# Performance work log

Measured on AMD Instinct MI355X. Metric: run time of the kernel, lower is better.

The kernel has to match this reference:

```python
import jax, jax.numpy as jnp
import numpy as np

EMBED_DIM = 2048
NUM_HEADS = 16
HEAD_DIM = EMBED_DIM // NUM_HEADS  # 128


def setup_inputs() -> dict:
    key = jax.random.key(0)
    ks = jax.random.split(key, 11)
    B, S, D, Hd = 2, 2048, EMBED_DIM, HEAD_DIM
    s_in = 1.0 / np.sqrt(D)
    return {
        "query": jax.random.normal(ks[0], (B, S, D), dtype=jnp.float32),
        "key": jax.random.normal(ks[1], (B, S, D), dtype=jnp.float32),
        "value": jax.random.normal(ks[2], (B, S, D), dtype=jnp.float32),
        "Wq": jax.random.normal(ks[3], (D, D), dtype=jnp.float32) * s_in,
        "bq": jax.random.normal(ks[4], (D,), dtype=jnp.float32) * s_in,
        "Wk": jax.random.normal(ks[5], (D, Hd), dtype=jnp.float32) * s_in,
        "bk": jax.random.normal(ks[6], (Hd,), dtype=jnp.float32) * s_in,
        "Wv": jax.random.normal(ks[7], (D, Hd), dtype=jnp.float32) * s_in,
        "bv": jax.random.normal(ks[8], (Hd,), dtype=jnp.float32) * s_in,
        "Wo": jax.random.normal(ks[9], (D, D), dtype=jnp.float32) * s_in,
        "bo": jax.random.normal(ks[10], (D,), dtype=jnp.float32) * s_in,
    }


def reference(query, key, value, Wq, bq, Wk, bk, Wv, bv, Wo, bo):
    B, S, D = query.shape
    H, Hd = NUM_HEADS, HEAD_DIM
    # projections
    Q = (query @ Wq + bq).reshape(B, S, H, Hd).transpose(0, 2, 1, 3)  # [B,H,S,Hd]
    K = key @ Wk + bk    # [B,S,Hd] single shared KV head
    V = value @ Wv + bv  # [B,S,Hd]
    scale = 1.0 / jnp.sqrt(jnp.asarray(Hd, dtype=Q.dtype))
    # MQA: broadcast single K/V head across H query heads
    scores = jnp.einsum("bhsd,btd->bhst", Q, K) * scale  # [B,H,S,S]
    attn = jax.nn.softmax(scores, axis=-1)
    out = jnp.einsum("bhst,btd->bhsd", attn, V)  # [B,H,S,Hd]
    out = out.transpose(0, 2, 1, 3).reshape(B, S, D)
    return out @ Wo + bo
```

## Files before the change

kernel.cpp:

```cpp
#include <hip/hip_runtime.h>
#include <stdint.h>

#define S_LEN 2048
#define EMBED 2048
#define NHEADS 16
#define HDIM 128

typedef __attribute__((ext_vector_type(8))) short bf16x8;
typedef __attribute__((ext_vector_type(4))) float f32x4;
typedef unsigned short us;

static __device__ __forceinline__ us f2b(float f) {
    union { float f; unsigned u; } x; x.f = f;
    unsigned r = x.u + 0x7fffu + ((x.u >> 16) & 1u);
    return (us)(r >> 16);
}

static __device__ __forceinline__ uint2 pack4(float a, float b, float c, float d) {
    uint2 u;
    u.x = (unsigned)f2b(a) | ((unsigned)f2b(b) << 16);
    u.y = (unsigned)f2b(c) | ((unsigned)f2b(d) << 16);
    return u;
}

static __device__ __forceinline__ void gl_lds16(const void* g, void* l) {
    __builtin_amdgcn_global_load_lds(
        (const __attribute__((address_space(1))) void*)g,
        (__attribute__((address_space(3))) void*)l, 16, 0, 0);
}


static __device__ __forceinline__ void dma_tile(const us* __restrict__ g, int k0,
                                                us* dst, int tid) {
#pragma unroll
    for (int i = 0; i < 4; i++) {
        int sl = i * 256 + tid;
        int row = sl >> 3, cp = sl & 7, c = cp ^ (row & 7);
        gl_lds16(g + (size_t)row * 2048 + k0 + c * 8,
                 (char*)dst + (i * 256 + (tid & 192)) * 16);
    }
}

static __device__ __forceinline__ void loadA_f32(const float* __restrict__ g,
                                                 float4 pf[8]) {
#pragma unroll
    for (int i = 0; i < 8; i++) pf[i] = ((const float4*)g)[i];
}

static __device__ __forceinline__ void writeA_f32(us* dst, const float4 pf[8],
                                                  int row, int h) {
#pragma unroll
    for (int cc = 0; cc < 4; cc++) {
        int p = (h * 4 + cc) ^ (row & 7);
        float4 a = pf[cc * 2], b = pf[cc * 2 + 1];
        uint4 u;
        u.x = (unsigned)f2b(a.x) | ((unsigned)f2b(a.y) << 16);
        u.y = (unsigned)f2b(a.z) | ((unsigned)f2b(a.w) << 16);
        u.z = (unsigned)f2b(b.x) | ((unsigned)f2b(b.y) << 16);
        u.w = (unsigned)f2b(b.z) | ((unsigned)f2b(b.w) << 16);
        *(uint4*)&dst[row * 64 + p * 8] = u;
    }
}

static __device__ __forceinline__ void frag_mfma(const us* curA, const us* curB,
                                                 int wm, int wn, int lm, int quad,
                                                 f32x4 acc[4][4]) {
#pragma unroll
    for (int kc = 0; kc < 2; kc++) {
        bf16x8 af[4], bfr[4];
#pragma unroll
        for (int mi = 0; mi < 4; mi++) {
            int row = wm * 64 + mi * 16 + lm;
            int p = (kc * 4 + quad) ^ (row & 7);
            af[mi] = *(const bf16x8*)&curA[row * 64 + p * 8];
        }
#pragma unroll
        for (int ni = 0; ni < 4; ni++) {
            int row = wn * 64 + ni * 16 + lm;
            int p = (kc * 4 + quad) ^ (row & 7);
            bfr[ni] = *(const bf16x8*)&curB[row * 64 + p * 8];
        }
#pragma unroll
        for (int mi = 0; mi < 4; mi++)
#pragma unroll
            for (int ni = 0; ni < 4; ni++)
                acc[mi][ni] = __builtin_amdgcn_mfma_f32_16x16x32_bf16(
                    af[mi], bfr[ni], acc[mi][ni], 0, 0, 0);
    }
}

__global__ void tcast3(const float* __restrict__ Wq, const float* __restrict__ Wk,
                       const float* __restrict__ Wv, const float* __restrict__ query,
                       us* __restrict__ Wqt, us* __restrict__ Wkvt,
                       us* __restrict__ qbf) {
    int b = blockIdx.x;
    if (b >= 2304) {
        int id = (b - 2304) * 256 + threadIdx.x;
        const float4* in4 = (const float4*)query;
        float4 a = in4[id * 2], c = in4[id * 2 + 1];
        uint4 u;
        u.x = (unsigned)f2b(a.x) | ((unsigned)f2b(a.y) << 16);
        u.y = (unsigned)f2b(a.z) | ((unsigned)f2b(a.w) << 16);
        u.z = (unsigned)f2b(c.x) | ((unsigned)f2b(c.y) << 16);
        u.w = (unsigned)f2b(c.z) | ((unsigned)f2b(c.w) << 16);
        ((uint4*)qbf)[id] = u;
        return;
    }
    const float* in; us* out; int N, rel;
    if (b < 2048)      { in = Wq; out = Wqt;  N = 2048; rel = b; }
    else if (b < 2176) { in = Wk; out = Wkvt; N = 128;  rel = b - 2048; }
    else               { in = Wv; out = Wkvt + (size_t)128 * 2048; N = 128; rel = b - 2176; }
    int id = rel * 256 + threadIdx.x;
    int n = id & (N - 1), k0 = (id / N) * 8;
    us t8[8];
#pragma unroll
    for (int j = 0; j < 8; j++) t8[j] = f2b(in[(size_t)(k0 + j) * N + n]);
    *(uint4*)&out[(size_t)n * 2048 + k0] = *(uint4*)t8;
}

__global__ __launch_bounds__(256, 2) void proj_qkv(
    const float* __restrict__ key, const float* __restrict__ value,
    const us* __restrict__ qbf, const us* __restrict__ Wqt,
    const us* __restrict__ Wkvt, const float* __restrict__ bq,
    us* __restrict__ Qh, float* __restrict__ part)
{
    __shared__ __align__(16) us A0[128 * 64], A1[128 * 64];
    __shared__ __align__(16) us B0[128 * 64], B1[128 * 64];

    const int tid = threadIdx.x;
    const int lane = tid & 63, w = tid >> 6, lm = lane & 15, quad = lane >> 4;
    const int wm = w >> 1, wn = w & 1;
    const int id = blockIdx.x;

    f32x4 acc[4][4];
#pragma unroll
    for (int i = 0; i < 4; i++)
#pragma unroll
        for (int j = 0; j < 4; j++) acc[i][j] = (f32x4){0.f, 0.f, 0.f, 0.f};

    if (id < 512) {
        const int bn = (id & 15) * 128, bm = (id >> 4) * 128;
        const us* Atile = qbf + (size_t)bm * 2048;
        const us* Btile = Wqt + (size_t)bn * 2048;

        dma_tile(Atile, 0, A0, tid);
        dma_tile(Btile, 0, B0, tid);

        for (int kk = 0; kk < 32; kk += 2) {
            __syncthreads();
            if (kk + 1 < 32) { dma_tile(Atile, (kk + 1) * 64, A1, tid);
                               dma_tile(Btile, (kk + 1) * 64, B1, tid); }
            frag_mfma(A0, B0, wm, wn, lm, quad, acc);
            __syncthreads();
            if (kk + 2 < 32) { dma_tile(Atile, (kk + 2) * 64, A0, tid);
                               dma_tile(Btile, (kk + 2) * 64, B0, tid); }
            frag_mfma(A1, B1, wm, wn, lm, quad, acc);
        }

#pragma unroll
        for (int mi = 0; mi < 4; mi++)
#pragma unroll
            for (int ni = 0; ni < 4; ni++) {
                int col = bn + wn * 64 + ni * 16 + lm;
                float bv = bq[col];
#pragma unroll
                for (int r = 0; r < 4; r++) {
                    int row = bm + wm * 64 + mi * 16 + quad * 4 + r;
                    float v = acc[mi][ni][r] + bv;
                    int b = row >> 11, s = row & 2047;
                    int hh = col >> 7, hd = col & 127;
                    size_t addr = (((size_t)(b * 16 + hh) * 2048 + s) << 7)
                                  + (((hd >> 3) ^ (s & 7)) << 3) + (hd & 7);
                    Qh[addr] = f2b(v);
                }
            }
    } else {
        int e = id - 512;
        int z = e >> 6, r = e & 63, isV = r & 1;
        int bm = (r >> 1) * 128, bn = isV * 128;
        const float* Atile = (isV ? value : key) + (size_t)bm * 2048;
        const us* Btile = Wkvt + (size_t)bn * 2048;
        const int kbeg = z * 512, iters = 8;
        const int arow = tid >> 1, h = tid & 1;
        const float* Ag = Atile + (size_t)arow * 2048 + h * 32;

        float4 pf[8];
        loadA_f32(Ag + kbeg, pf);
        dma_tile(Btile, kbeg, B0, tid);
        writeA_f32(A0, pf, arow, h);

        for (int kk = 0; kk < iters; kk += 2) {
            const int k1 = kbeg + (kk + 1) * 64;
            const int k2 = kbeg + (kk + 2) * 64;
            __syncthreads();
            if (kk + 1 < iters) { loadA_f32(Ag + k1, pf); dma_tile(Btile, k1, B1, tid); }
            frag_mfma(A0, B0, wm, wn, lm, quad, acc);
            if (kk + 1 < iters) writeA_f32(A1, pf, arow, h);
            __syncthreads();
            if (kk + 2 < iters) { loadA_f32(Ag + k2, pf); dma_tile(Btile, k2, B0, tid); }
            frag_mfma(A1, B1, wm, wn, lm, quad, acc);
            if (kk + 2 < iters) writeA_f32(A0, pf, arow, h);
        }

        float* pp = part + (size_t)z * 1048576;
#pragma unroll
        for (int mi = 0; mi < 4; mi++)
#pragma unroll
            for (int ni = 0; ni < 4; ni++) {
                int col = bn + wn * 64 + ni * 16 + lm;
#pragma unroll
                for (int r = 0; r < 4; r++) {
                    int row = bm + wm * 64 + mi * 16 + quad * 4 + r;
                    pp[(size_t)row * 256 + col] = acc[mi][ni][r];
                }
            }
    }
}

__global__ void finish_wot(const float* __restrict__ part, const float* __restrict__ bk,
                           const float* __restrict__ bv, us* __restrict__ Kb,
                           us* __restrict__ Vt, const float* __restrict__ Wo,
                           us* __restrict__ Wot) {
    int b = blockIdx.x;
    if (b < 2048) {
        int id = b * 256 + threadIdx.x;
        int n = id & 2047, k0 = (id >> 11) * 8;
        us t8[8];
#pragma unroll
        for (int j = 0; j < 8; j++) t8[j] = f2b(Wo[(size_t)(k0 + j) * 2048 + n]);
        *(uint4*)&Wot[(size_t)n * 2048 + k0] = *(uint4*)t8;
    } else {
        int id = (b - 2048) * 256 + threadIdx.x;
        int row = id >> 8, n = id & 255;
        float s = part[id] + part[1048576 + id] + part[2097152 + id] + part[3145728 + id];
        int bb = row >> 11, t = row & 2047;
        if (n < 128) {
            int hd = n;
            s += bk[hd];
            Kb[((size_t)(bb * 2048 + t) << 7) + (((hd >> 3) ^ (t & 7)) << 3) + (hd & 7)] = f2b(s);
        } else {
            int hd = n - 128;
            s += bv[hd];
            size_t addr = (((size_t)(bb * 64 + (t >> 5)) * 128 + hd) << 5)
                          + ((((t >> 3) & 3) ^ ((hd >> 1) & 3)) << 3) + (t & 7);
            Vt[addr] = f2b(s);
        }
    }
}

__global__ __launch_bounds__(256, 2) void mqa_attn(
    const us* __restrict__ Qh, const us* __restrict__ Kb,
    const us* __restrict__ Vt, us* __restrict__ AO)
{
    __shared__ __align__(16) char smem[65536];
    us* Qs  = (us*)smem;
    us* Ksb = (us*)(smem + 32768);
    us* Vts = (us*)(smem + 49152);
    us* Ps  = (us*)(smem + 57344);
    float* Lb = (float*)(smem + 32768);

    const int tid  = threadIdx.x;
    const int lane = tid & 63;
    const int w    = tid >> 6;
    const int lm   = lane & 15;
    const int quad = lane >> 4;
    const int wm = w >> 1, wn = w & 1;
    const int q0 = blockIdx.x * 128;
    const int h  = blockIdx.y;
    const int b  = blockIdx.z;
    const float sc = 0.08838834764831845f;

    const us* Qtile = Qh + (((size_t)(b * 16 + h) * 2048 + q0) << 7);
    const us* Kbase = Kb + ((size_t)b * 2048 << 7);
    const us* Vbase = Vt + (size_t)b * 64 * 4096;

#pragma unroll
    for (int i = 0; i < 8; i++) {
        int sl = w * 512 + i * 64 + lane;
        gl_lds16(Qtile + sl * 8, smem + (w * 512 + i * 64) * 16);
    }
#pragma unroll
    for (int i = 0; i < 2; i++) {
        int sl = w * 128 + i * 64 + lane;
        gl_lds16(Kbase + sl * 8, (char*)Ksb + (w * 128 + i * 64) * 16);
        gl_lds16(Vbase + sl * 8, (char*)Vts + (w * 128 + i * 64) * 16);
    }
    __syncthreads();

    bf16x8 qf[4][4];
#pragma unroll
    for (int nt = 0; nt < 4; nt++)
#pragma unroll
        for (int ks = 0; ks < 4; ks++) {
            int q = wn * 64 + nt * 16 + lm;
            int cp = (ks * 4 + quad) ^ (q & 7);
            qf[nt][ks] = *(const bf16x8*)&Qs[q * 128 + cp * 8];
        }

    f32x4 oacc[4][4];
#pragma unroll
    for (int i = 0; i < 4; i++)
#pragma unroll
        for (int j = 0; j < 4; j++) oacc[i][j] = (f32x4){0.f, 0.f, 0.f, 0.f};
    float lsum[4] = {0.f, 0.f, 0.f, 0.f};

    for (int it = 0; it < 64; ++it) {
        const int p = it & 1;
        const us* Kst = Ksb + p * 4096;

        f32x4 sacc[4];
#pragma unroll
        for (int nt = 0; nt < 4; nt++) sacc[nt] = (f32x4){0.f, 0.f, 0.f, 0.f};
#pragma unroll
        for (int ks = 0; ks < 4; ks++) {
            int t = wm * 16 + lm;
            int cp = (ks * 4 + quad) ^ (lm & 7);
            bf16x8 kf = *(const bf16x8*)&Kst[t * 128 + cp * 8];
#pragma unroll
            for (int nt = 0; nt < 4; nt++)
                sacc[nt] = __builtin_amdgcn_mfma_f32_16x16x32_bf16(
                    kf, qf[nt][ks], sacc[nt], 0, 0, 0);
        }
        if (it < 63) {
            const us* kg = Kbase + (it + 1) * 32 * 128;
#pragma unroll
            for (int i = 0; i < 2; i++) {
                int sl = w * 128 + i * 64 + lane;
                gl_lds16(kg + sl * 8, (char*)Ksb + (1 - p) * 8192 + (w * 128 + i * 64) * 16);
            }
        }
#pragma unroll
        for (int nt = 0; nt < 4; nt++) {
            int q = wn * 64 + nt * 16 + lm;
            float p0 = __expf(sacc[nt][0] * sc);
            float p1 = __expf(sacc[nt][1] * sc);
            float p2 = __expf(sacc[nt][2] * sc);
            float p3 = __expf(sacc[nt][3] * sc);
            lsum[nt] += (p0 + p1) + (p2 + p3);
            int tb = wm * 16 + quad * 4;
            int cp = (tb >> 3) ^ ((q >> 1) & 3);
            *(uint2*)&Ps[q * 32 + cp * 8 + (tb & 7)] = pack4(p0, p1, p2, p3);
        }
        __syncthreads();

        bf16x8 vf[4], pfr[4];
#pragma unroll
        for (int mt = 0; mt < 4; mt++) {
            int hd = (wm * 4 + mt) * 16 + lm;
            int cp = quad ^ ((hd >> 1) & 3);
            vf[mt] = *(const bf16x8*)&Vts[hd * 32 + cp * 8];
        }
#pragma unroll
        for (int nt = 0; nt < 4; nt++) {
            int q = (wn * 4 + nt) * 16 + lm;
            int cp = quad ^ ((q >> 1) & 3);
            pfr[nt] = *(const bf16x8*)&Ps[q * 32 + cp * 8];
        }
#pragma unroll
        for (int mt = 0; mt < 4; mt++)
#pragma unroll
            for (int nt = 0; nt < 4; nt++)
                oacc[mt][nt] = __builtin_amdgcn_mfma_f32_16x16x32_bf16(
                    vf[mt], pfr[nt], oacc[mt][nt], 0, 0, 0);
        __syncthreads();

        if (it < 63) {
            const us* vg = Vbase + (it + 1) * 4096;
#pragma unroll
            for (int i = 0; i < 2; i++) {
                int sl = w * 128 + i * 64 + lane;
                gl_lds16(vg + sl * 8, (char*)Vts + (w * 128 + i * 64) * 16);
            }
        }
    }

#pragma unroll
    for (int nt = 0; nt < 4; nt++) {
        lsum[nt] += __shfl_xor(lsum[nt], 16);
        lsum[nt] += __shfl_xor(lsum[nt], 32);
    }
    if (quad == 0) {
#pragma unroll
        for (int nt = 0; nt < 4; nt++)
            Lb[wm * 128 + wn * 64 + nt * 16 + lm] = lsum[nt];
    }
    __syncthreads();

#pragma unroll
    for (int nt = 0; nt < 4; nt++) {
        int q = (wn * 4 + nt) * 16 + lm;
        float linv = 1.f / (Lb[q] + Lb[128 + q]);
#pragma unroll
        for (int mt = 0; mt < 4; mt++) {
            int hdb = (wm * 4 + mt) * 16 + quad * 4;
            uint2 u = pack4(oacc[mt][nt][0] * linv, oacc[mt][nt][1] * linv,
                            oacc[mt][nt][2] * linv, oacc[mt][nt][3] * linv);
            *(uint2*)&AO[((size_t)(b * 2048 + q0 + q)) * 2048 + h * 128 + hdb] = u;
        }
    }
}

__global__ __launch_bounds__(256, 2) void oproj(
    const us* __restrict__ AO, const us* __restrict__ Wot,
    const float* __restrict__ bo, float* __restrict__ out)
{
    __shared__ __align__(16) us A0[128 * 64], A1[128 * 64];
    __shared__ __align__(16) us B0[128 * 64], B1[128 * 64];

    const int tid = threadIdx.x;
    const int lane = tid & 63, w = tid >> 6, lm = lane & 15, quad = lane >> 4;
    const int wm = w >> 1, wn = w & 1;
    const int bn = blockIdx.x * 128, bm = blockIdx.y * 128;
    const us* Atile = AO + (size_t)bm * 2048;
    const us* Btile = Wot + (size_t)bn * 2048;

    f32x4 acc[4][4];
#pragma unroll
    for (int i = 0; i < 4; i++)
#pragma unroll
        for (int j = 0; j < 4; j++) acc[i][j] = (f32x4){0.f, 0.f, 0.f, 0.f};

    dma_tile(Atile, 0, A0, tid);
    dma_tile(Btile, 0, B0, tid);

    for (int kk = 0; kk < 32; kk += 2) {
        __syncthreads();
        if (kk + 1 < 32) { dma_tile(Atile, (kk + 1) * 64, A1, tid);
                           dma_tile(Btile, (kk + 1) * 64, B1, tid); }
        frag_mfma(A0, B0, wm, wn, lm, quad, acc);
        __syncthreads();
        if (kk + 2 < 32) { dma_tile(Atile, (kk + 2) * 64, A0, tid);
                           dma_tile(Btile, (kk + 2) * 64, B0, tid); }
        frag_mfma(A1, B1, wm, wn, lm, quad, acc);
    }

#pragma unroll
    for (int mi = 0; mi < 4; mi++)
#pragma unroll
        for (int ni = 0; ni < 4; ni++) {
            int col = bn + wn * 64 + ni * 16 + lm;
            float bv = bo[col];
#pragma unroll
            for (int r = 0; r < 4; r++) {
                int row = bm + wm * 64 + mi * 16 + quad * 4 + r;
                out[(size_t)row * 2048 + col] = acc[mi][ni][r] + bv;
            }
        }
}

extern "C" void kernel_launch(void* const* d_in, const int* in_sizes, int n_in,
                              void* d_out, int out_size, void* d_ws, size_t ws_size,
                              hipStream_t stream) {
    const float* query = (const float*)d_in[0];
    const float* key   = (const float*)d_in[1];
    const float* value = (const float*)d_in[2];
    const float* Wq = (const float*)d_in[3];
    const float* bq = (const float*)d_in[4];
    const float* Wk = (const float*)d_in[5];
    const float* bk = (const float*)d_in[6];
    const float* Wv = (const float*)d_in[7];
    const float* bv = (const float*)d_in[8];
    const float* Wo = (const float*)d_in[9];
    const float* bo = (const float*)d_in[10];
    float* out = (float*)d_out;

    char* ws = (char*)d_ws;
    us*    Wqt  = (us*)ws;
    us*    Wot  = Wqt;
    us*    Wkvt = (us*)(ws + 8388608);
    us*    Qh   = (us*)(ws + 9437184);
    float* part = (float*)(ws + 26214400);
    us*    AO   = (us*)part;
    us*    Kb   = (us*)(ws + 42991616);
    us*    Vtb  = (us*)(ws + 44040192);
    us*    qbf  = (us*)(ws + 45088768);

    dim3 blk(256);
    tcast3<<<6400, blk, 0, stream>>>(Wq, Wk, Wv, query, Wqt, Wkvt, qbf);
    proj_qkv<<<768, blk, 0, stream>>>(key, value, qbf, Wqt, Wkvt, bq, Qh, part);
    finish_wot<<<6144, blk, 0, stream>>>(part, bk, bv, Kb, Vtb, Wo, Wot);
    mqa_attn<<<dim3(16, 16, 2), blk, 0, stream>>>(Qh, Kb, Vtb, AO);
    oproj<<<dim3(16, 32), blk, 0, stream>>>(AO, Wot, bo, out);
}
```

Baseline: 358.6 us.

## Double-buffer V and P tiles, drop per-iteration barrier, use exp2 and packed bf16

The attention loop now double-buffers the V and P shared-memory tiles and places P over the Q staging area, which is freed by a new barrier after the Q fragments are loaded. This removes the second __syncthreads per iteration. The K prefetch is issued at the top of each iteration, and both MFMA phases are wrapped with s_setprio to favour matrix issue. The softmax exponent uses a raw v_exp_f32 with log2e folded into the scale, and bf16 packing uses the hardware v_cvt_pk_bf16_f32 instruction. The main risks are subtler cross-wave hazards on the reused buffers and the lack of range handling in the raw exp instruction.

```diff
diff --git a/kernel.cpp b/kernel.cpp
--- a/kernel.cpp
+++ b/kernel.cpp
@@ -16,11 +16,23 @@
     return (us)(r >> 16);
 }
 
+static __device__ __forceinline__ unsigned cvtpk(float a, float b) {
+    unsigned r;
+    asm("v_cvt_pk_bf16_f32 %0, %1, %2" : "=v"(r) : "v"(a), "v"(b));
+    return r;
+}
+
 static __device__ __forceinline__ uint2 pack4(float a, float b, float c, float d) {
     uint2 u;
-    u.x = (unsigned)f2b(a) | ((unsigned)f2b(b) << 16);
-    u.y = (unsigned)f2b(c) | ((unsigned)f2b(d) << 16);
+    u.x = cvtpk(a, b);
+    u.y = cvtpk(c, d);
     return u;
+}
+
+static __device__ __forceinline__ float fexp2(float x) {
+    float r;
+    asm("v_exp_f32 %0, %1" : "=v"(r) : "v"(x));
+    return r;
 }
 
 static __device__ __forceinline__ void gl_lds16(const void* g, void* l) {
@@ -254,9 +266,9 @@
 {
     __shared__ __align__(16) char smem[65536];
     us* Qs  = (us*)smem;
+    us* Ps  = (us*)smem;
     us* Ksb = (us*)(smem + 32768);
     us* Vts = (us*)(smem + 49152);
-    us* Ps  = (us*)(smem + 57344);
     float* Lb = (float*)(smem + 32768);
 
     const int tid  = threadIdx.x;
@@ -268,7 +280,7 @@
     const int q0 = blockIdx.x * 128;
     const int h  = blockIdx.y;
     const int b  = blockIdx.z;
-    const float sc = 0.08838834764831845f;
+    const float C = 0.12751743150179665f;
 
     const us* Qtile = Qh + (((size_t)(b * 16 + h) * 2048 + q0) << 7);
     const us* Kbase = Kb + ((size_t)b * 2048 << 7);
@@ -296,6 +308,7 @@
             int cp = (ks * 4 + quad) ^ (q & 7);
             qf[nt][ks] = *(const bf16x8*)&Qs[q * 128 + cp * 8];
         }
+    __syncthreads();
 
     f32x4 oacc[4][4];
 #pragma unroll
@@ -308,9 +321,19 @@
         const int p = it & 1;
         const us* Kst = Ksb + p * 4096;
 
+        if (it < 63) {
+            const us* kg = Kbase + (it + 1) * 4096;
+#pragma unroll
+            for (int i = 0; i < 2; i++) {
+                int sl = w * 128 + i * 64 + lane;
+                gl_lds16(kg + sl * 8, (char*)Ksb + (1 - p) * 8192 + (w * 128 + i * 64) * 16);
+            }
+        }
+
         f32x4 sacc[4];
 #pragma unroll
         for (int nt = 0; nt < 4; nt++) sacc[nt] = (f32x4){0.f, 0.f, 0.f, 0.f};
+        __builtin_amdgcn_s_setprio(1);
 #pragma unroll
         for (int ks = 0; ks < 4; ks++) {
             int t = wm * 16 + lm;
@@ -321,55 +344,54 @@
                 sacc[nt] = __builtin_amdgcn_mfma_f32_16x16x32_bf16(
                     kf, qf[nt][ks], sacc[nt], 0, 0, 0);
         }
-        if (it < 63) {
-            const us* kg = Kbase + (it + 1) * 32 * 128;
-#pragma unroll
-            for (int i = 0; i < 2; i++) {
-                int sl = w * 128 + i * 64 + lane;
-                gl_lds16(kg + sl * 8, (char*)Ksb + (1 - p) * 8192 + (w * 128 + i * 64) * 16);
-            }
-        }
+        __builtin_amdgcn_s_setprio(0);
+
+        us* Pw = Ps + p * 4096;
 #pragma unroll
         for (int nt = 0; nt < 4; nt++) {
             int q = wn * 64 + nt * 16 + lm;
-            float p0 = __expf(sacc[nt][0] * sc);
-            float p1 = __expf(sacc[nt][1] * sc);
-            float p2 = __expf(sacc[nt][2] * sc);
-            float p3 = __expf(sacc[nt][3] * sc);
+            float p0 = fexp2(sacc[nt][0] * C);
+            float p1 = fexp2(sacc[nt][1] * C);
+            float p2 = fexp2(sacc[nt][2] * C);
+            float p3 = fexp2(sacc[nt][3] * C);
             lsum[nt] += (p0 + p1) + (p2 + p3);
             int tb = wm * 16 + quad * 4;
             int cp = (tb >> 3) ^ ((q >> 1) & 3);
-            *(uint2*)&Ps[q * 32 + cp * 8 + (tb & 7)] = pack4(p0, p1, p2, p3);
-        }
+            *(uint2*)&Pw[q * 32 + cp * 8 + (tb & 7)] = pack4(p0, p1, p2, p3);
+        }
+
         __syncthreads();
 
+        const us* Vst = Vts + p * 4096;
+        const us* Pr = Ps + p * 4096;
         bf16x8 vf[4], pfr[4];
 #pragma unroll
         for (int mt = 0; mt < 4; mt++) {
             int hd = (wm * 4 + mt) * 16 + lm;
             int cp = quad ^ ((hd >> 1) & 3);
-            vf[mt] = *(const bf16x8*)&Vts[hd * 32 + cp * 8];
+            vf[mt] = *(const bf16x8*)&Vst[hd * 32 + cp * 8];
         }
 #pragma unroll
         for (int nt = 0; nt < 4; nt++) {
             int q = (wn * 4 + nt) * 16 + lm;
             int cp = quad ^ ((q >> 1) & 3);
-            pfr[nt] = *(const bf16x8*)&Ps[q * 32 + cp * 8];
-        }
+            pfr[nt] = *(const bf16x8*)&Pr[q * 32 + cp * 8];
+        }
+        __builtin_amdgcn_s_setprio(1);
 #pragma unroll
         for (int mt = 0; mt < 4; mt++)
 #pragma unroll
             for (int nt = 0; nt < 4; nt++)
                 oacc[mt][nt] = __builtin_amdgcn_mfma_f32_16x16x32_bf16(
                     vf[mt], pfr[nt], oacc[mt][nt], 0, 0, 0);
-        __syncthreads();
+        __builtin_amdgcn_s_setprio(0);
 
         if (it < 63) {
             const us* vg = Vbase + (it + 1) * 4096;
 #pragma unroll
             for (int i = 0; i < 2; i++) {
                 int sl = w * 128 + i * 64 + lane;
-                gl_lds16(vg + sl * 8, (char*)Vts + (w * 128 + i * 64) * 16);
+                gl_lds16(vg + sl * 8, (char*)Vts + (1 - p) * 8192 + (w * 128 + i * 64) * 16);
             }
         }
     }
```

New measurement: 336.6 us. 6.1% less time.
